# Kernel optimization log

Measured on AMD Instinct MI355X. Metric: run time of the kernel, lower is better.

Reference implementation:

```python
import jax, jax.numpy as jnp
import numpy as np

D_MODEL = 1024
NHEAD = 16
HEAD_DIM = D_MODEL // NHEAD
D_FF = 4096
B, S = 2, 2048
LN_EPS = 1e-5


def _linear_params(key, d_out, d_in):
    kw, kb = jax.random.split(key)
    lim = 1.0 / np.sqrt(d_in)
    W = jax.random.uniform(kw, (d_out, d_in), jnp.float32, -lim, lim)
    b = jax.random.uniform(kb, (d_out,), jnp.float32, -lim, lim)
    return W, b


def setup_inputs() -> dict:
    key = jax.random.key(0)
    ks = jax.random.split(key, 8)
    src = jax.random.normal(ks[0], (B, S, D_MODEL), jnp.float32)
    mask = jax.random.randint(ks[1], (B, S), 0, 2).astype(bool)
    Wq, bq = _linear_params(ks[2], D_MODEL, D_MODEL)
    Wk, bk = _linear_params(ks[3], D_MODEL, D_MODEL)
    Wv, bv = _linear_params(ks[4], D_MODEL, D_MODEL)
    Wo, bo = _linear_params(ks[5], D_MODEL, D_MODEL)
    W1, b1 = _linear_params(ks[6], D_FF, D_MODEL)
    W2, b2 = _linear_params(ks[7], D_MODEL, D_FF)
    ln1_g = jnp.ones((D_MODEL,), jnp.float32)
    ln1_b = jnp.zeros((D_MODEL,), jnp.float32)
    ln2_g = jnp.ones((D_MODEL,), jnp.float32)
    ln2_b = jnp.zeros((D_MODEL,), jnp.float32)
    return dict(src=src, mask=mask, Wq=Wq, bq=bq, Wk=Wk, bk=bk, Wv=Wv, bv=bv,
                Wo=Wo, bo=bo, W1=W1, b1=b1, W2=W2, b2=b2,
                ln1_g=ln1_g, ln1_b=ln1_b, ln2_g=ln2_g, ln2_b=ln2_b)


def _layernorm(x, g, b):
    mu = jnp.mean(x, axis=-1, keepdims=True)
    var = jnp.mean(jnp.square(x - mu), axis=-1, keepdims=True)
    return (x - mu) * jax.lax.rsqrt(var + LN_EPS) * g + b


def reference(src, mask, Wq, bq, Wk, bk, Wv, bv, Wo, bo, W1, b1, W2, b2,
              ln1_g, ln1_b, ln2_g, ln2_b):
    batch, seq, _ = src.shape
    src_norm = _layernorm(src, ln1_g, ln1_b)
    # projections (torch Linear: x @ W.T + b), split heads -> [B,H,S,Dh]
    def proj(W, b):
        y = jnp.einsum('bsi,oi->bso', src_norm, W) + b
        return y.reshape(batch, seq, NHEAD, HEAD_DIM).transpose(0, 2, 1, 3)
    q, k, v = proj(Wq, bq), proj(Wk, bk), proj(Wv, bv)
    scores = jnp.einsum('bhqd,bhkd->bhqk', q, k) / np.sqrt(HEAD_DIM)
    scores = jnp.where(mask[:, None, None, :], -10000.0, scores)
    attn_probs = jax.nn.softmax(scores, axis=-1)
    attn_out = jnp.einsum('bhqk,bhkd->bhqd', attn_probs, v)
    attn_out = attn_out.transpose(0, 2, 1, 3).reshape(batch, seq, D_MODEL)
    attn_out = jnp.einsum('bsi,oi->bso', attn_out, Wo) + bo
    src = src + attn_out
    src_norm2 = _layernorm(src, ln2_g, ln2_b)
    h = jax.nn.relu(jnp.einsum('bsi,oi->bso', src_norm2, W1) + b1)
    ff = jnp.einsum('bsi,oi->bso', h, W2) + b2
    src = src + ff
    return (src, attn_probs)
```

## Files before the change

kernel.cpp:

```cpp
#include <hip/hip_runtime.h>
#include <math.h>

typedef __bf16 bf16;
typedef __bf16 bf16x4 __attribute__((ext_vector_type(4)));
typedef __bf16 bf16x8 __attribute__((ext_vector_type(8)));
typedef float f32x4 __attribute__((ext_vector_type(4)));

__device__ __forceinline__ f32x4 mfma16(bf16x8 a, bf16x8 b, f32x4 c) {
  return __builtin_amdgcn_mfma_f32_16x16x32_bf16(a, b, c, 0, 0, 0);
}

__device__ __forceinline__ void gload_lds16(const void* g, void* l) {
  __builtin_amdgcn_global_load_lds((__attribute__((address_space(1))) void*)(g),
                                   (__attribute__((address_space(3))) void*)(l),
                                   16, 0, 0);
}

__global__ __launch_bounds__(256)
void cvt_all(const float* __restrict__ Wq, const float* __restrict__ Wk,
             const float* __restrict__ Wv, const float* __restrict__ Wo,
             const float* __restrict__ W1, const float* __restrict__ W2,
             const float* __restrict__ bq, const float* __restrict__ bk,
             const float* __restrict__ bv, bf16* __restrict__ wqkv,
             bf16* __restrict__ wob, bf16* __restrict__ w1b,
             bf16* __restrict__ w2b, float* __restrict__ bqkv) {
  const int i = blockIdx.x * 256 + threadIdx.x;
  if (i < 3145728) {
    float4 v;
    bf16* dst;
    size_t di;
    if (i < 262144) { v = ((const float4*)Wq)[i]; dst = wqkv; di = i; }
    else if (i < 524288) { v = ((const float4*)Wk)[i - 262144]; dst = wqkv; di = i; }
    else if (i < 786432) { v = ((const float4*)Wv)[i - 524288]; dst = wqkv; di = i; }
    else if (i < 1048576) { v = ((const float4*)Wo)[i - 786432]; dst = wob; di = i - 786432; }
    else if (i < 2097152) { v = ((const float4*)W1)[i - 1048576]; dst = w1b; di = i - 1048576; }
    else { v = ((const float4*)W2)[i - 2097152]; dst = w2b; di = i - 2097152; }
    bf16x4 o;
    o[0] = (bf16)v.x; o[1] = (bf16)v.y; o[2] = (bf16)v.z; o[3] = (bf16)v.w;
    reinterpret_cast<bf16x4*>(dst)[di] = o;
  } else {
    const int j = i - 3145728;
    const float* s = (j < 256) ? bq : ((j < 512) ? bk : bv);
    reinterpret_cast<float4*>(bqkv)[j] = reinterpret_cast<const float4*>(s)[j & 255];
  }
}

__global__ __launch_bounds__(256)
void ln_bf16(const float* __restrict__ x, const float* __restrict__ g,
             const float* __restrict__ bta, bf16* __restrict__ y) {
  const int row = blockIdx.x, t = threadIdx.x;
  const float4 v = reinterpret_cast<const float4*>(x)[(size_t)row * 256 + t];
  float s1 = v.x + v.y + v.z + v.w;
  float s2 = v.x * v.x + v.y * v.y + v.z * v.z + v.w * v.w;
#pragma unroll
  for (int m = 1; m < 64; m <<= 1) {
    s1 += __shfl_xor(s1, m);
    s2 += __shfl_xor(s2, m);
  }
  __shared__ float red[8];
  if ((t & 63) == 0) { red[(t >> 6) * 2] = s1; red[(t >> 6) * 2 + 1] = s2; }
  __syncthreads();
  s1 = red[0] + red[2] + red[4] + red[6];
  s2 = red[1] + red[3] + red[5] + red[7];
  const float mu = s1 * (1.f / 1024.f);
  const float rs = rsqrtf(s2 * (1.f / 1024.f) - mu * mu + 1e-5f);
  const float4 gv = reinterpret_cast<const float4*>(g)[t];
  const float4 bv = reinterpret_cast<const float4*>(bta)[t];
  bf16x4 o;
  o[0] = (bf16)((v.x - mu) * rs * gv.x + bv.x);
  o[1] = (bf16)((v.y - mu) * rs * gv.y + bv.y);
  o[2] = (bf16)((v.z - mu) * rs * gv.z + bv.z);
  o[3] = (bf16)((v.w - mu) * rs * gv.w + bv.w);
  reinterpret_cast<bf16x4*>(y)[(size_t)row * 256 + t] = o;
}

__global__ __launch_bounds__(256)
void tr_v(const bf16* __restrict__ QKV, bf16* __restrict__ VT) {
  __shared__ bf16 T[64 * 80];
  const int t = threadIdx.x;
  const int sb = blockIdx.x * 64, h = blockIdx.y, b = blockIdx.z;
  const int srow = t >> 2, c16 = t & 3;
  const bf16* src = QKV + (size_t)(b * 2048 + sb + srow) * 3072 + 2048 + h * 64 + c16 * 16;
  bf16x8 a0 = *reinterpret_cast<const bf16x8*>(src);
  bf16x8 a1 = *reinterpret_cast<const bf16x8*>(src + 8);
  *reinterpret_cast<bf16x8*>(&T[srow * 80 + c16 * 16]) = a0;
  *reinterpret_cast<bf16x8*>(&T[srow * 80 + c16 * 16 + 8]) = a1;
  __syncthreads();
  const int drow = t >> 2, sq = t & 3;
  bf16x8 o0, o1;
#pragma unroll
  for (int j = 0; j < 8; ++j) o0[j] = T[(sq * 16 + j) * 80 + drow];
#pragma unroll
  for (int j = 0; j < 8; ++j) o1[j] = T[(sq * 16 + 8 + j) * 80 + drow];
  bf16* dst = VT + ((size_t)(b * 16 + h) * 64 + drow) * 2048 + sb + sq * 16;
  *reinterpret_cast<bf16x8*>(dst) = o0;
  *reinterpret_cast<bf16x8*>(dst + 8) = o1;
}

template <bool RELU, bool QSC>
__global__ __launch_bounds__(512)
void gemm_bt3(const bf16* __restrict__ A, const bf16* __restrict__ Bw,
              const float* __restrict__ bias, bf16* __restrict__ Cout,
              int M, int N, int K) {
  __shared__ bf16 As[3][128 * 32];
  __shared__ bf16 Bs[3][256 * 32];
  const int t = threadIdx.x, wave = t >> 6, lane = t & 63;
  const int l15 = lane & 15, lhi = lane >> 4;
  const int nwg = gridDim.x * gridDim.y;
  const int orig = blockIdx.y * gridDim.x + blockIdx.x;
  const int wgid = (orig & 7) * (nwg >> 3) + (orig >> 3);
  const int bx = wgid % gridDim.x, by = wgid / gridDim.x;
  const int m0 = by * 128, n0 = bx * 256;
  const int wm = (wave >> 2) * 64, wn = (wave & 3) * 64;
  const f32x4 z4 = {0.f, 0.f, 0.f, 0.f};
  f32x4 acc[4][4];
#pragma unroll
  for (int m = 0; m < 4; ++m)
#pragma unroll
    for (int n = 0; n < 4; ++n) acc[m][n] = z4;

  const int da = t * 16;
  const int ra = da >> 6, ca = (da & 63) ^ ((ra & 3) << 4);
  const bf16* agp = A + (size_t)(m0 + ra) * K + (ca >> 1);
  int db_[2], rb_[2];
  const bf16* bgp[2];
#pragma unroll
  for (int j = 0; j < 2; ++j) {
    db_[j] = j * 8192 + t * 16;
    rb_[j] = db_[j] >> 6;
    const int cb = (db_[j] & 63) ^ ((rb_[j] & 3) << 4);
    bgp[j] = Bw + (size_t)(n0 + rb_[j]) * K + (cb >> 1);
  }

#define G3_STAGE(k0, bb)                                                      \
  do {                                                                        \
    gload_lds16(agp + (k0), (char*)As[bb] + da);                              \
    gload_lds16(bgp[0] + (k0), (char*)Bs[bb] + db_[0]);                       \
    gload_lds16(bgp[1] + (k0), (char*)Bs[bb] + db_[1]);                       \
  } while (0)

  const int nt = K >> 5;
  G3_STAGE(0, 0);
  G3_STAGE(32, 1);
  asm volatile("s_waitcnt vmcnt(3)" ::: "memory");
  __builtin_amdgcn_s_barrier();

  for (int kt = 0; kt < nt; ++kt) {
    if (kt + 2 < nt) G3_STAGE((kt + 2) * 32, (kt + 2) % 3);
    const char* Ac = (const char*)As[kt % 3];
    const char* Bc = (const char*)Bs[kt % 3];
    bf16x8 af[4], bfr[4];
#pragma unroll
    for (int m = 0; m < 4; ++m) {
      const int row = wm + m * 16 + l15;
      af[m] = *reinterpret_cast<const bf16x8*>(
          Ac + row * 64 + ((lhi * 16) ^ ((row & 3) << 4)));
    }
#pragma unroll
    for (int n = 0; n < 4; ++n) {
      const int row = wn + n * 16 + l15;
      bfr[n] = *reinterpret_cast<const bf16x8*>(
          Bc + row * 64 + ((lhi * 16) ^ ((row & 3) << 4)));
    }
    __builtin_amdgcn_s_setprio(1);
#pragma unroll
    for (int m = 0; m < 4; ++m)
#pragma unroll
      for (int n = 0; n < 4; ++n) acc[m][n] = mfma16(af[m], bfr[n], acc[m][n]);
    __builtin_amdgcn_s_setprio(0);
    if (kt + 1 < nt) {
      if (kt + 2 < nt)
        asm volatile("s_waitcnt vmcnt(3)" ::: "memory");
      else
        asm volatile("s_waitcnt vmcnt(0)" ::: "memory");
      __builtin_amdgcn_s_barrier();
    }
  }
#undef G3_STAGE

  const float sc = (QSC && n0 < 1024) ? 0.18033688011112042f : 1.0f;
#pragma unroll
  for (int m = 0; m < 4; ++m) {
    const int row_base = m0 + wm + m * 16 + lhi * 4;
#pragma unroll
    for (int n = 0; n < 4; ++n) {
      const int col = n0 + wn + n * 16 + l15;
      const float bv = bias[col];
#pragma unroll
      for (int r = 0; r < 4; ++r) {
        float v = (acc[m][n][r] + bv) * sc;
        if (RELU) v = v > 0.f ? v : 0.f;
        Cout[(size_t)(row_base + r) * N + col] = (bf16)v;
      }
    }
  }
}

template <int TM, bool OUT_BF16, bool RELU, bool RES, bool QSC>
__global__ __launch_bounds__(256)
void gemm_bt(const bf16* __restrict__ A, const bf16* __restrict__ Bw,
             const float* __restrict__ bias, const float* __restrict__ res,
             void* __restrict__ Cout, int M, int N, int K) {
  constexpr int MR = TM / 32;
  constexpr int ACH = TM / 64;
  __shared__ bf16 As[3][TM * 32];
  __shared__ bf16 Bs[3][128 * 32];
  const int t = threadIdx.x, wave = t >> 6, lane = t & 63;
  const int l15 = lane & 15, lhi = lane >> 4;
  const int nwg = gridDim.x * gridDim.y;
  const int orig = blockIdx.y * gridDim.x + blockIdx.x;
  const int wgid = (orig & 7) * (nwg >> 3) + (orig >> 3);
  const int bx = wgid % gridDim.x, by = wgid / gridDim.x;
  const int m0 = by * TM, n0 = bx * 128;
  const int wm = (wave >> 1) * (TM / 2), wn = (wave & 1) * 64;
  const f32x4 z4 = {0.f, 0.f, 0.f, 0.f};
  f32x4 acc[MR][4];
#pragma unroll
  for (int m = 0; m < MR; ++m)
#pragma unroll
    for (int n = 0; n < 4; ++n) acc[m][n] = z4;

  int soff[2], srow[2], scol[2];
#pragma unroll
  for (int i = 0; i < 2; ++i) {
    soff[i] = (i * 4 + wave) * 1024 + lane * 16;
    srow[i] = soff[i] >> 6;
    scol[i] = (soff[i] & 63) >> 1;
  }

#define GEMM_STAGE(k0, bb)                                                    \
  do {                                                                        \
    _Pragma("unroll")                                                         \
    for (int i = 0; i < ACH; ++i)                                             \
      gload_lds16(A + (size_t)(m0 + srow[i]) * K + (k0) + scol[i],            \
                  (char*)As[bb] + soff[i]);                                   \
    _Pragma("unroll")                                                         \
    for (int i = 0; i < 2; ++i)                                               \
      gload_lds16(Bw + (size_t)(n0 + srow[i]) * K + (k0) + scol[i],           \
                  (char*)Bs[bb] + soff[i]);                                   \
  } while (0)

  const int nt = K >> 5;
  GEMM_STAGE(0, 0);
  GEMM_STAGE(32, 1);
  if constexpr (TM == 128)
    asm volatile("s_waitcnt vmcnt(4)" ::: "memory");
  else
    asm volatile("s_waitcnt vmcnt(3)" ::: "memory");
  __builtin_amdgcn_s_barrier();

  for (int kt = 0; kt < nt; ++kt) {
    if (kt + 2 < nt) GEMM_STAGE((kt + 2) * 32, (kt + 2) % 3);
    const bf16* Ac = As[kt % 3];
    const bf16* Bc = Bs[kt % 3];
    bf16x8 af[MR], bfr[4];
#pragma unroll
    for (int m = 0; m < MR; ++m)
      af[m] = *reinterpret_cast<const bf16x8*>(&Ac[(wm + m * 16 + l15) * 32 + lhi * 8]);
#pragma unroll
    for (int n = 0; n < 4; ++n)
      bfr[n] = *reinterpret_cast<const bf16x8*>(&Bc[(wn + n * 16 + l15) * 32 + lhi * 8]);
    __builtin_amdgcn_s_setprio(1);
#pragma unroll
    for (int m = 0; m < MR; ++m)
#pragma unroll
      for (int n = 0; n < 4; ++n) acc[m][n] = mfma16(af[m], bfr[n], acc[m][n]);
    __builtin_amdgcn_s_setprio(0);
    if (kt + 1 < nt) {
      if (kt + 2 < nt) {
        if constexpr (TM == 128)
          asm volatile("s_waitcnt vmcnt(4)" ::: "memory");
        else
          asm volatile("s_waitcnt vmcnt(3)" ::: "memory");
      } else {
        asm volatile("s_waitcnt vmcnt(0)" ::: "memory");
      }
      __builtin_amdgcn_s_barrier();
    }
  }
#undef GEMM_STAGE

  const float sc = (QSC && n0 < 1024) ? 0.18033688011112042f : 1.0f;
#pragma unroll
  for (int m = 0; m < MR; ++m) {
    const int row_base = m0 + wm + m * 16 + lhi * 4;
#pragma unroll
    for (int n = 0; n < 4; ++n) {
      const int col = n0 + wn + n * 16 + l15;
      const float bv = bias[col];
#pragma unroll
      for (int r = 0; r < 4; ++r) {
        const int row = row_base + r;
        float v = (acc[m][n][r] + bv) * sc;
        if (RELU) v = v > 0.f ? v : 0.f;
        if (RES) v += res[(size_t)row * N + col];
        if (OUT_BF16)
          ((bf16*)Cout)[(size_t)row * N + col] = (bf16)v;
        else
          ((float*)Cout)[(size_t)row * N + col] = v;
      }
    }
  }
}

__global__ __launch_bounds__(512)
void attn_fused2(const bf16* __restrict__ Qp, const bf16* __restrict__ Kp,
                 const bf16* __restrict__ VTp, const int* __restrict__ mask,
                 float* __restrict__ probs, bf16* __restrict__ Ob) {
  constexpr int S = 2048, LD = 3072, KB = 128, NT = S / KB;
  __shared__ bf16 Kt[KB * 64];
  __shared__ bf16 Vt[64 * KB];
  __shared__ bf16 P[128 * KB];
  __shared__ float msk2[2][KB];
  const int t = threadIdx.x, wave = t >> 6, lane = t & 63;
  const int l15 = lane & 15, lhi = lane >> 4;
  const int flat = blockIdx.x + 16 * (blockIdx.y + 16 * blockIdx.z);
  const int wg = (flat & 7) * 64 + (flat >> 3);
  const int q0 = (wg & 15) * 128, h = (wg >> 4) & 15, b = wg >> 8;
  const int* mrow = mask + b * S;
  const f32x4 z4 = {0.f, 0.f, 0.f, 0.f};

  const bf16* kgp[2];
  const bf16* vgp[2];
  int soff[2];
#pragma unroll
  for (int i = 0; i < 2; ++i) {
    const int off = (i * 8 + wave) * 1024 + lane * 16;
    soff[i] = off;
    const int krow = off >> 7, kbin = off & 127;
    kgp[i] = Kp + (size_t)(b * S + krow) * LD + h * 64 + ((kbin ^ ((krow & 7) << 4)) >> 1);
    const int d = off >> 8, vbin = off & 255;
    vgp[i] = VTp + (size_t)((b * 16 + h) * 64 + d) * S + ((vbin ^ ((d & 7) << 4)) >> 1);
  }

  bf16x8 qf[2];
#pragma unroll
  for (int ks = 0; ks < 2; ++ks)
    qf[ks] = *reinterpret_cast<const bf16x8*>(
        Qp + (size_t)(b * S + q0 + wave * 16 + l15) * LD + h * 64 + ks * 32 + lhi * 8);

  bf16x8 kreg[2];
  float mnext;
#pragma unroll
  for (int i = 0; i < 2; ++i) kreg[i] = *reinterpret_cast<const bf16x8*>(kgp[i]);
  mnext = (t < KB) ? (mrow[t] ? 0.f : 1.f) : 0.f;
#pragma unroll
  for (int i = 0; i < 2; ++i)
    *reinterpret_cast<bf16x8*>((char*)Kt + soff[i]) = kreg[i];
  if (t < KB) msk2[0][t] = mnext;
  __syncthreads();

  float lpart = 0.f;
  for (int kt = 0; kt < NT; ++kt) {
    const int kv0 = kt * KB;
    if (kt + 1 < NT) {
#pragma unroll
      for (int i = 0; i < 2; ++i)
        kreg[i] = *reinterpret_cast<const bf16x8*>(kgp[i] + (size_t)(kv0 + KB) * LD);
      mnext = (t < KB) ? (mrow[kv0 + KB + t] ? 0.f : 1.f) : 0.f;
    }
    const char* kb = (kt & 1) ? (const char*)Vt : (const char*)Kt;
    const float* mc = msk2[kt & 1];
    f32x4 sa[8];
#pragma unroll
    for (int n = 0; n < 8; ++n) sa[n] = z4;
    __builtin_amdgcn_s_setprio(1);
#pragma unroll
    for (int ks = 0; ks < 2; ++ks)
#pragma unroll
      for (int n = 0; n < 8; ++n) {
        const int krow = n * 16 + l15;
        bf16x8 kf = *reinterpret_cast<const bf16x8*>(
            kb + krow * 128 + ((ks * 64 + lhi * 16) ^ ((krow & 7) << 4)));
        sa[n] = mfma16(kf, qf[ks], sa[n]);
      }
    __builtin_amdgcn_s_setprio(0);
#pragma unroll
    for (int n = 0; n < 8; ++n)
#pragma unroll
      for (int r = 0; r < 4; ++r)
        lpart += __builtin_exp2f(sa[n][r]) * mc[n * 16 + lhi * 4 + r];
    if (kt + 1 < NT) {
      char* kbn = ((kt + 1) & 1) ? (char*)Vt : (char*)Kt;
#pragma unroll
      for (int i = 0; i < 2; ++i)
        *reinterpret_cast<bf16x8*>(kbn + soff[i]) = kreg[i];
      if (t < KB) msk2[(kt + 1) & 1][t] = mnext;
    }
    __syncthreads();
  }
  lpart += __shfl_xor(lpart, 16);
  lpart += __shfl_xor(lpart, 32);
  const float il = 1.f / lpart;

  f32x4 oa[4];
#pragma unroll
  for (int n = 0; n < 4; ++n) oa[n] = z4;
  float* pbase = probs + ((size_t)(b * 16 + h) * S + q0 + wave * 16 + l15) * S;
  const int prw = wave * 16 + l15;

  bf16x8 vreg[2];
#pragma unroll
  for (int i = 0; i < 2; ++i) {
    kreg[i] = *reinterpret_cast<const bf16x8*>(kgp[i]);
    vreg[i] = *reinterpret_cast<const bf16x8*>(vgp[i]);
  }
  mnext = (t < KB) ? (mrow[t] ? 0.f : 1.f) : 0.f;
#pragma unroll
  for (int i = 0; i < 2; ++i) {
    *reinterpret_cast<bf16x8*>((char*)Kt + soff[i]) = kreg[i];
    *reinterpret_cast<bf16x8*>((char*)Vt + soff[i]) = vreg[i];
  }
  if (t < KB) msk2[0][t] = mnext;
  __syncthreads();

  for (int kt = 0; kt < NT; ++kt) {
    const int kv0 = kt * KB;
    if (kt + 1 < NT) {
#pragma unroll
      for (int i = 0; i < 2; ++i) {
        kreg[i] = *reinterpret_cast<const bf16x8*>(kgp[i] + (size_t)(kv0 + KB) * LD);
        vreg[i] = *reinterpret_cast<const bf16x8*>(vgp[i] + kv0 + KB);
      }
      mnext = (t < KB) ? (mrow[kv0 + KB + t] ? 0.f : 1.f) : 0.f;
    }

    f32x4 sa[8];
#pragma unroll
    for (int n = 0; n < 8; ++n) sa[n] = z4;
    __builtin_amdgcn_s_setprio(1);
#pragma unroll
    for (int ks = 0; ks < 2; ++ks)
#pragma unroll
      for (int n = 0; n < 8; ++n) {
        const int krow = n * 16 + l15;
        bf16x8 kf = *reinterpret_cast<const bf16x8*>(
            (char*)Kt + krow * 128 + ((ks * 64 + lhi * 16) ^ ((krow & 7) << 4)));
        sa[n] = mfma16(kf, qf[ks], sa[n]);
      }
    __builtin_amdgcn_s_setprio(0);

#pragma unroll
    for (int n = 0; n < 8; ++n) {
      f32x4 praw, pn;
#pragma unroll
      for (int r = 0; r < 4; ++r) {
        praw[r] = __builtin_exp2f(sa[n][r]) * msk2[0][n * 16 + lhi * 4 + r];
        pn[r] = praw[r] * il;
      }
      __builtin_nontemporal_store(pn, reinterpret_cast<f32x4*>(pbase + kv0 + n * 16 + lhi * 4));
      bf16x4 pb;
      pb[0] = (bf16)praw[0]; pb[1] = (bf16)praw[1];
      pb[2] = (bf16)praw[2]; pb[3] = (bf16)praw[3];
      *reinterpret_cast<bf16x4*>(
          (char*)P + prw * 256 + ((n * 32 + lhi * 8) ^ ((prw & 7) << 4))) = pb;
    }
    __builtin_amdgcn_s_setprio(1);
#pragma unroll
    for (int ks = 0; ks < 4; ++ks) {
      bf16x8 pf = *reinterpret_cast<const bf16x8*>(
          (char*)P + prw * 256 + ((ks * 64 + lhi * 16) ^ ((prw & 7) << 4)));
#pragma unroll
      for (int nn = 0; nn < 4; ++nn) {
        const int vr = nn * 16 + l15;
        bf16x8 vf = *reinterpret_cast<const bf16x8*>(
            (char*)Vt + vr * 256 + ((ks * 64 + lhi * 16) ^ ((vr & 7) << 4)));
        oa[nn] = mfma16(pf, vf, oa[nn]);
      }
    }
    __builtin_amdgcn_s_setprio(0);
    __syncthreads();
    if (kt + 1 < NT) {
#pragma unroll
      for (int i = 0; i < 2; ++i) {
        *reinterpret_cast<bf16x8*>((char*)Kt + soff[i]) = kreg[i];
        *reinterpret_cast<bf16x8*>((char*)Vt + soff[i]) = vreg[i];
      }
      if (t < KB) msk2[0][t] = mnext;
    }
    __syncthreads();
  }

  float il4[4];
#pragma unroll
  for (int r = 0; r < 4; ++r) il4[r] = __shfl(il, lhi * 4 + r);
#pragma unroll
  for (int nn = 0; nn < 4; ++nn)
#pragma unroll
    for (int r = 0; r < 4; ++r)
      Ob[(size_t)(b * S + q0 + wave * 16 + lhi * 4 + r) * 1024 + h * 64 + nn * 16 + l15] =
          (bf16)(oa[nn][r] * il4[r]);
}

extern "C" void kernel_launch(void* const* d_in, const int* in_sizes, int n_in,
                              void* d_out, int out_size, void* d_ws, size_t ws_size,
                              hipStream_t stream) {
  const float* src = (const float*)d_in[0];
  const int* mask = (const int*)d_in[1];
  const float* Wq = (const float*)d_in[2];
  const float* bq = (const float*)d_in[3];
  const float* Wk = (const float*)d_in[4];
  const float* bk = (const float*)d_in[5];
  const float* Wv = (const float*)d_in[6];
  const float* bv = (const float*)d_in[7];
  const float* Wo = (const float*)d_in[8];
  const float* bo = (const float*)d_in[9];
  const float* W1 = (const float*)d_in[10];
  const float* b1 = (const float*)d_in[11];
  const float* W2 = (const float*)d_in[12];
  const float* b2 = (const float*)d_in[13];
  const float* ln1g = (const float*)d_in[14];
  const float* ln1b = (const float*)d_in[15];
  const float* ln2g = (const float*)d_in[16];
  const float* ln2b = (const float*)d_in[17];

  float* out0 = (float*)d_out;
  float* probs = (float*)d_out + (size_t)4194304;

  char* w = (char*)d_ws;
  const size_t MB = 1u << 20;
  bf16* wqkv = (bf16*)(w);
  bf16* wob = (bf16*)(w + 6 * MB);
  bf16* w1b = (bf16*)(w + 8 * MB);
  bf16* w2b = (bf16*)(w + 16 * MB);
  bf16* xn = (bf16*)(w + 24 * MB);
  bf16* QKV = (bf16*)(w + 32 * MB);
  bf16* Ob = (bf16*)(w + 56 * MB);
  bf16* hb = (bf16*)(w + 32 * MB);
  bf16* VT = (bf16*)(w + 64 * MB);
  float* s2 = (float*)(w + 64 * MB);
  float* bqkv = (float*)(w + 80 * MB);

  cvt_all<<<12291, 256, 0, stream>>>(Wq, Wk, Wv, Wo, W1, W2, bq, bk, bv,
                                     wqkv, wob, w1b, w2b, bqkv);

  ln_bf16<<<4096, 256, 0, stream>>>(src, ln1g, ln1b, xn);
  gemm_bt3<false, true><<<dim3(12, 32), 512, 0, stream>>>(
      xn, wqkv, bqkv, QKV, 4096, 3072, 1024);
  tr_v<<<dim3(32, 16, 2), 256, 0, stream>>>(QKV, VT);
  attn_fused2<<<dim3(16, 16, 2), 512, 0, stream>>>(
      QKV, QKV + 1024, VT, mask, probs, Ob);
  gemm_bt<64, false, false, true, false><<<dim3(8, 64), 256, 0, stream>>>(
      Ob, wob, bo, src, s2, 4096, 1024, 1024);
  ln_bf16<<<4096, 256, 0, stream>>>(s2, ln2g, ln2b, xn);
  gemm_bt3<true, false><<<dim3(16, 32), 512, 0, stream>>>(
      xn, w1b, b1, hb, 4096, 4096, 1024);
  gemm_bt<64, false, false, true, false><<<dim3(8, 64), 256, 0, stream>>>(
      hb, w2b, b2, s2, out0, 4096, 1024, 4096);

  (void)in_sizes; (void)n_in; (void)out_size; (void)ws_size;
}
```

Measured before the change: 408.6 us.

## Switch GEMMs to 32x32 MFMA, fuse LN1 into prep, store residual as bf16

Both GEMM kernels move from 16x16x32 to 32x32x16 bf16 MFMA tiles, which cuts LDS fragment reads per MFMA and changes the epilogue row mapping. The first layernorm is merged into the weight-conversion launch to save one kernel launch. The intermediate residual after attention is now stored as bf16 rather than fp32, which halves its traffic but loses precision in the residual path that feeds the final output.

```diff
diff --git a/kernel.cpp b/kernel.cpp
--- a/kernel.cpp
+++ b/kernel.cpp
@@ -5,9 +5,13 @@
 typedef __bf16 bf16x4 __attribute__((ext_vector_type(4)));
 typedef __bf16 bf16x8 __attribute__((ext_vector_type(8)));
 typedef float f32x4 __attribute__((ext_vector_type(4)));
+typedef float f32x16 __attribute__((ext_vector_type(16)));
 
 __device__ __forceinline__ f32x4 mfma16(bf16x8 a, bf16x8 b, f32x4 c) {
   return __builtin_amdgcn_mfma_f32_16x16x32_bf16(a, b, c, 0, 0, 0);
+}
+__device__ __forceinline__ f32x16 mfma32(bf16x8 a, bf16x8 b, f32x16 c) {
+  return __builtin_amdgcn_mfma_f32_32x32x16_bf16(a, b, c, 0, 0, 0);
 }
 
 __device__ __forceinline__ void gload_lds16(const void* g, void* l) {
@@ -17,39 +21,75 @@
 }
 
 __global__ __launch_bounds__(256)
-void cvt_all(const float* __restrict__ Wq, const float* __restrict__ Wk,
-             const float* __restrict__ Wv, const float* __restrict__ Wo,
-             const float* __restrict__ W1, const float* __restrict__ W2,
-             const float* __restrict__ bq, const float* __restrict__ bk,
-             const float* __restrict__ bv, bf16* __restrict__ wqkv,
-             bf16* __restrict__ wob, bf16* __restrict__ w1b,
-             bf16* __restrict__ w2b, float* __restrict__ bqkv) {
-  const int i = blockIdx.x * 256 + threadIdx.x;
-  if (i < 3145728) {
-    float4 v;
-    bf16* dst;
-    size_t di;
-    if (i < 262144) { v = ((const float4*)Wq)[i]; dst = wqkv; di = i; }
-    else if (i < 524288) { v = ((const float4*)Wk)[i - 262144]; dst = wqkv; di = i; }
-    else if (i < 786432) { v = ((const float4*)Wv)[i - 524288]; dst = wqkv; di = i; }
-    else if (i < 1048576) { v = ((const float4*)Wo)[i - 786432]; dst = wob; di = i - 786432; }
-    else if (i < 2097152) { v = ((const float4*)W1)[i - 1048576]; dst = w1b; di = i - 1048576; }
-    else { v = ((const float4*)W2)[i - 2097152]; dst = w2b; di = i - 2097152; }
+void prep(const float* __restrict__ Wq, const float* __restrict__ Wk,
+          const float* __restrict__ Wv, const float* __restrict__ Wo,
+          const float* __restrict__ W1, const float* __restrict__ W2,
+          const float* __restrict__ bq, const float* __restrict__ bk,
+          const float* __restrict__ bv, bf16* __restrict__ wqkv,
+          bf16* __restrict__ wob, bf16* __restrict__ w1b,
+          bf16* __restrict__ w2b, float* __restrict__ bqkv,
+          const float* __restrict__ src, const float* __restrict__ g,
+          const float* __restrict__ bta, bf16* __restrict__ y) {
+  __shared__ float red[8];
+  if (blockIdx.x < 12291) {
+    const int i = blockIdx.x * 256 + threadIdx.x;
+    if (i < 3145728) {
+      float4 v;
+      bf16* dst;
+      size_t di;
+      if (i < 262144) { v = ((const float4*)Wq)[i]; dst = wqkv; di = i; }
+      else if (i < 524288) { v = ((const float4*)Wk)[i - 262144]; dst = wqkv; di = i; }
+      else if (i < 786432) { v = ((const float4*)Wv)[i - 524288]; dst = wqkv; di = i; }
+      else if (i < 1048576) { v = ((const float4*)Wo)[i - 786432]; dst = wob; di = i - 786432; }
+      else if (i < 2097152) { v = ((const float4*)W1)[i - 1048576]; dst = w1b; di = i - 1048576; }
+      else { v = ((const float4*)W2)[i - 2097152]; dst = w2b; di = i - 2097152; }
+      bf16x4 o;
+      o[0] = (bf16)v.x; o[1] = (bf16)v.y; o[2] = (bf16)v.z; o[3] = (bf16)v.w;
+      reinterpret_cast<bf16x4*>(dst)[di] = o;
+    } else {
+      const int j = i - 3145728;
+      const float* s = (j < 256) ? bq : ((j < 512) ? bk : bv);
+      reinterpret_cast<float4*>(bqkv)[j] = reinterpret_cast<const float4*>(s)[j & 255];
+    }
+  } else {
+    const int row = blockIdx.x - 12291, t = threadIdx.x;
+    const float4 v = reinterpret_cast<const float4*>(src)[(size_t)row * 256 + t];
+    float s1 = v.x + v.y + v.z + v.w;
+    float s2 = v.x * v.x + v.y * v.y + v.z * v.z + v.w * v.w;
+#pragma unroll
+    for (int m = 1; m < 64; m <<= 1) {
+      s1 += __shfl_xor(s1, m);
+      s2 += __shfl_xor(s2, m);
+    }
+    if ((t & 63) == 0) { red[(t >> 6) * 2] = s1; red[(t >> 6) * 2 + 1] = s2; }
+    __syncthreads();
+    s1 = red[0] + red[2] + red[4] + red[6];
+    s2 = red[1] + red[3] + red[5] + red[7];
+    const float mu = s1 * (1.f / 1024.f);
+    const float rs = rsqrtf(s2 * (1.f / 1024.f) - mu * mu + 1e-5f);
+    const float4 gv = reinterpret_cast<const float4*>(g)[t];
+    const float4 bv = reinterpret_cast<const float4*>(bta)[t];
     bf16x4 o;
-    o[0] = (bf16)v.x; o[1] = (bf16)v.y; o[2] = (bf16)v.z; o[3] = (bf16)v.w;
-    reinterpret_cast<bf16x4*>(dst)[di] = o;
+    o[0] = (bf16)((v.x - mu) * rs * gv.x + bv.x);
+    o[1] = (bf16)((v.y - mu) * rs * gv.y + bv.y);
+    o[2] = (bf16)((v.z - mu) * rs * gv.z + bv.z);
+    o[3] = (bf16)((v.w - mu) * rs * gv.w + bv.w);
+    reinterpret_cast<bf16x4*>(y)[(size_t)row * 256 + t] = o;
+  }
+}
+
+template <bool INBF>
+__global__ __launch_bounds__(256)
+void ln_any(const void* __restrict__ xx, const float* __restrict__ g,
+            const float* __restrict__ bta, bf16* __restrict__ y) {
+  const int row = blockIdx.x, t = threadIdx.x;
+  float4 v;
+  if constexpr (INBF) {
+    bf16x4 bv4 = reinterpret_cast<const bf16x4*>(xx)[(size_t)row * 256 + t];
+    v.x = (float)bv4[0]; v.y = (float)bv4[1]; v.z = (float)bv4[2]; v.w = (float)bv4[3];
   } else {
-    const int j = i - 3145728;
-    const float* s = (j < 256) ? bq : ((j < 512) ? bk : bv);
-    reinterpret_cast<float4*>(bqkv)[j] = reinterpret_cast<const float4*>(s)[j & 255];
-  }
-}
-
-__global__ __launch_bounds__(256)
-void ln_bf16(const float* __restrict__ x, const float* __restrict__ g,
-             const float* __restrict__ bta, bf16* __restrict__ y) {
-  const int row = blockIdx.x, t = threadIdx.x;
-  const float4 v = reinterpret_cast<const float4*>(x)[(size_t)row * 256 + t];
+    v = reinterpret_cast<const float4*>(xx)[(size_t)row * 256 + t];
+  }
   float s1 = v.x + v.y + v.z + v.w;
   float s2 = v.x * v.x + v.y * v.y + v.z * v.z + v.w * v.w;
 #pragma unroll
@@ -105,31 +145,32 @@
   __shared__ bf16 As[3][128 * 32];
   __shared__ bf16 Bs[3][256 * 32];
   const int t = threadIdx.x, wave = t >> 6, lane = t & 63;
-  const int l15 = lane & 15, lhi = lane >> 4;
+  const int l31 = lane & 31, lh2 = lane >> 5;
   const int nwg = gridDim.x * gridDim.y;
   const int orig = blockIdx.y * gridDim.x + blockIdx.x;
   const int wgid = (orig & 7) * (nwg >> 3) + (orig >> 3);
   const int bx = wgid % gridDim.x, by = wgid / gridDim.x;
   const int m0 = by * 128, n0 = bx * 256;
   const int wm = (wave >> 2) * 64, wn = (wave & 3) * 64;
-  const f32x4 z4 = {0.f, 0.f, 0.f, 0.f};
-  f32x4 acc[4][4];
-#pragma unroll
-  for (int m = 0; m < 4; ++m)
-#pragma unroll
-    for (int n = 0; n < 4; ++n) acc[m][n] = z4;
+  f32x16 acc[2][2];
+#pragma unroll
+  for (int m = 0; m < 2; ++m)
+#pragma unroll
+    for (int n = 0; n < 2; ++n)
+#pragma unroll
+      for (int r = 0; r < 16; ++r) acc[m][n][r] = 0.f;
 
   const int da = t * 16;
   const int ra = da >> 6, ca = (da & 63) ^ ((ra & 3) << 4);
   const bf16* agp = A + (size_t)(m0 + ra) * K + (ca >> 1);
-  int db_[2], rb_[2];
+  int db_[2];
   const bf16* bgp[2];
 #pragma unroll
   for (int j = 0; j < 2; ++j) {
     db_[j] = j * 8192 + t * 16;
-    rb_[j] = db_[j] >> 6;
-    const int cb = (db_[j] & 63) ^ ((rb_[j] & 3) << 4);
-    bgp[j] = Bw + (size_t)(n0 + rb_[j]) * K + (cb >> 1);
+    const int rb = db_[j] >> 6;
+    const int cb = (db_[j] & 63) ^ ((rb & 3) << 4);
+    bgp[j] = Bw + (size_t)(n0 + rb) * K + (cb >> 1);
   }
 
 #define G3_STAGE(k0, bb)                                                      \
@@ -149,24 +190,31 @@
     if (kt + 2 < nt) G3_STAGE((kt + 2) * 32, (kt + 2) % 3);
     const char* Ac = (const char*)As[kt % 3];
     const char* Bc = (const char*)Bs[kt % 3];
-    bf16x8 af[4], bfr[4];
-#pragma unroll
-    for (int m = 0; m < 4; ++m) {
-      const int row = wm + m * 16 + l15;
-      af[m] = *reinterpret_cast<const bf16x8*>(
-          Ac + row * 64 + ((lhi * 16) ^ ((row & 3) << 4)));
-    }
-#pragma unroll
-    for (int n = 0; n < 4; ++n) {
-      const int row = wn + n * 16 + l15;
-      bfr[n] = *reinterpret_cast<const bf16x8*>(
-          Bc + row * 64 + ((lhi * 16) ^ ((row & 3) << 4)));
+    bf16x8 af[2][2], bfr[2][2];
+#pragma unroll
+    for (int tm = 0; tm < 2; ++tm) {
+      const int row = wm + tm * 32 + l31;
+#pragma unroll
+      for (int kh = 0; kh < 2; ++kh)
+        af[tm][kh] = *reinterpret_cast<const bf16x8*>(
+            Ac + row * 64 + ((kh * 32 + lh2 * 16) ^ ((row & 3) << 4)));
+    }
+#pragma unroll
+    for (int tn = 0; tn < 2; ++tn) {
+      const int row = wn + tn * 32 + l31;
+#pragma unroll
+      for (int kh = 0; kh < 2; ++kh)
+        bfr[tn][kh] = *reinterpret_cast<const bf16x8*>(
+            Bc + row * 64 + ((kh * 32 + lh2 * 16) ^ ((row & 3) << 4)));
     }
     __builtin_amdgcn_s_setprio(1);
 #pragma unroll
-    for (int m = 0; m < 4; ++m)
-#pragma unroll
-      for (int n = 0; n < 4; ++n) acc[m][n] = mfma16(af[m], bfr[n], acc[m][n]);
+    for (int kh = 0; kh < 2; ++kh)
+#pragma unroll
+      for (int tm = 0; tm < 2; ++tm)
+#pragma unroll
+        for (int tn = 0; tn < 2; ++tn)
+          acc[tm][tn] = mfma32(af[tm][kh], bfr[tn][kh], acc[tm][tn]);
     __builtin_amdgcn_s_setprio(0);
     if (kt + 1 < nt) {
       if (kt + 2 < nt)
@@ -180,45 +228,42 @@
 
   const float sc = (QSC && n0 < 1024) ? 0.18033688011112042f : 1.0f;
 #pragma unroll
-  for (int m = 0; m < 4; ++m) {
-    const int row_base = m0 + wm + m * 16 + lhi * 4;
-#pragma unroll
-    for (int n = 0; n < 4; ++n) {
-      const int col = n0 + wn + n * 16 + l15;
+  for (int tm = 0; tm < 2; ++tm) {
+#pragma unroll
+    for (int tn = 0; tn < 2; ++tn) {
+      const int col = n0 + wn + tn * 32 + l31;
       const float bv = bias[col];
 #pragma unroll
-      for (int r = 0; r < 4; ++r) {
-        float v = (acc[m][n][r] + bv) * sc;
+      for (int reg = 0; reg < 16; ++reg) {
+        const int row = m0 + wm + tm * 32 + (reg & 3) + 8 * (reg >> 2) + 4 * lh2;
+        float v = (acc[tm][tn][reg] + bv) * sc;
         if (RELU) v = v > 0.f ? v : 0.f;
-        Cout[(size_t)(row_base + r) * N + col] = (bf16)v;
-      }
-    }
-  }
-}
-
-template <int TM, bool OUT_BF16, bool RELU, bool RES, bool QSC>
+        Cout[(size_t)row * N + col] = (bf16)v;
+      }
+    }
+  }
+}
+
+template <bool OUT_BF16, bool RES, bool RESBF>
 __global__ __launch_bounds__(256)
 void gemm_bt(const bf16* __restrict__ A, const bf16* __restrict__ Bw,
-             const float* __restrict__ bias, const float* __restrict__ res,
+             const float* __restrict__ bias, const void* __restrict__ res,
              void* __restrict__ Cout, int M, int N, int K) {
-  constexpr int MR = TM / 32;
-  constexpr int ACH = TM / 64;
-  __shared__ bf16 As[3][TM * 32];
+  __shared__ bf16 As[3][64 * 32];
   __shared__ bf16 Bs[3][128 * 32];
   const int t = threadIdx.x, wave = t >> 6, lane = t & 63;
-  const int l15 = lane & 15, lhi = lane >> 4;
+  const int l31 = lane & 31, lh2 = lane >> 5;
   const int nwg = gridDim.x * gridDim.y;
   const int orig = blockIdx.y * gridDim.x + blockIdx.x;
   const int wgid = (orig & 7) * (nwg >> 3) + (orig >> 3);
   const int bx = wgid % gridDim.x, by = wgid / gridDim.x;
-  const int m0 = by * TM, n0 = bx * 128;
-  const int wm = (wave >> 1) * (TM / 2), wn = (wave & 1) * 64;
-  const f32x4 z4 = {0.f, 0.f, 0.f, 0.f};
-  f32x4 acc[MR][4];
-#pragma unroll
-  for (int m = 0; m < MR; ++m)
-#pragma unroll
-    for (int n = 0; n < 4; ++n) acc[m][n] = z4;
+  const int m0 = by * 64, n0 = bx * 128;
+  const int wm = (wave >> 1) * 32, wn = (wave & 1) * 64;
+  f32x16 acc[2];
+#pragma unroll
+  for (int n = 0; n < 2; ++n)
+#pragma unroll
+    for (int r = 0; r < 16; ++r) acc[n][r] = 0.f;
 
   int soff[2], srow[2], scol[2];
 #pragma unroll
@@ -230,75 +275,71 @@
 
 #define GEMM_STAGE(k0, bb)                                                    \
   do {                                                                        \
-    _Pragma("unroll")                                                         \
-    for (int i = 0; i < ACH; ++i)                                             \
-      gload_lds16(A + (size_t)(m0 + srow[i]) * K + (k0) + scol[i],            \
-                  (char*)As[bb] + soff[i]);                                   \
-    _Pragma("unroll")                                                         \
-    for (int i = 0; i < 2; ++i)                                               \
-      gload_lds16(Bw + (size_t)(n0 + srow[i]) * K + (k0) + scol[i],           \
-                  (char*)Bs[bb] + soff[i]);                                   \
+    gload_lds16(A + (size_t)(m0 + srow[0]) * K + (k0) + scol[0],              \
+                (char*)As[bb] + soff[0]);                                     \
+    gload_lds16(Bw + (size_t)(n0 + srow[0]) * K + (k0) + scol[0],             \
+                (char*)Bs[bb] + soff[0]);                                     \
+    gload_lds16(Bw + (size_t)(n0 + srow[1]) * K + (k0) + scol[1],             \
+                (char*)Bs[bb] + soff[1]);                                     \
   } while (0)
 
   const int nt = K >> 5;
   GEMM_STAGE(0, 0);
   GEMM_STAGE(32, 1);
-  if constexpr (TM == 128)
-    asm volatile("s_waitcnt vmcnt(4)" ::: "memory");
-  else
-    asm volatile("s_waitcnt vmcnt(3)" ::: "memory");
+  asm volatile("s_waitcnt vmcnt(3)" ::: "memory");
   __builtin_amdgcn_s_barrier();
 
   for (int kt = 0; kt < nt; ++kt) {
     if (kt + 2 < nt) GEMM_STAGE((kt + 2) * 32, (kt + 2) % 3);
-    const bf16* Ac = As[kt % 3];
-    const bf16* Bc = Bs[kt % 3];
-    bf16x8 af[MR], bfr[4];
-#pragma unroll
-    for (int m = 0; m < MR; ++m)
-      af[m] = *reinterpret_cast<const bf16x8*>(&Ac[(wm + m * 16 + l15) * 32 + lhi * 8]);
-#pragma unroll
-    for (int n = 0; n < 4; ++n)
-      bfr[n] = *reinterpret_cast<const bf16x8*>(&Bc[(wn + n * 16 + l15) * 32 + lhi * 8]);
+    const char* Ac = (const char*)As[kt % 3];
+    const char* Bc = (const char*)Bs[kt % 3];
+    bf16x8 af[2], bfr[2][2];
+    {
+      const int row = wm + l31;
+#pragma unroll
+      for (int kh = 0; kh < 2; ++kh)
+        af[kh] = *reinterpret_cast<const bf16x8*>(Ac + row * 64 + kh * 32 + lh2 * 16);
+    }
+#pragma unroll
+    for (int tn = 0; tn < 2; ++tn) {
+      const int row = wn + tn * 32 + l31;
+#pragma unroll
+      for (int kh = 0; kh < 2; ++kh)
+        bfr[tn][kh] = *reinterpret_cast<const bf16x8*>(Bc + row * 64 + kh * 32 + lh2 * 16);
+    }
     __builtin_amdgcn_s_setprio(1);
 #pragma unroll
-    for (int m = 0; m < MR; ++m)
-#pragma unroll
-      for (int n = 0; n < 4; ++n) acc[m][n] = mfma16(af[m], bfr[n], acc[m][n]);
+    for (int kh = 0; kh < 2; ++kh)
+#pragma unroll
+      for (int tn = 0; tn < 2; ++tn)
+        acc[tn] = mfma32(af[kh], bfr[tn][kh], acc[tn]);
     __builtin_amdgcn_s_setprio(0);
     if (kt + 1 < nt) {
-      if (kt + 2 < nt) {
-        if constexpr (TM == 128)
-          asm volatile("s_waitcnt vmcnt(4)" ::: "memory");
-        else
-          asm volatile("s_waitcnt vmcnt(3)" ::: "memory");
-      } else {
+      if (kt + 2 < nt)
+        asm volatile("s_waitcnt vmcnt(3)" ::: "memory");
+      else
         asm volatile("s_waitcnt vmcnt(0)" ::: "memory");
-      }
       __builtin_amdgcn_s_barrier();
     }
   }
 #undef GEMM_STAGE
 
-  const float sc = (QSC && n0 < 1024) ? 0.18033688011112042f : 1.0f;
-#pragma unroll
-  for (int m = 0; m < MR; ++m) {
-    const int row_base = m0 + wm + m * 16 + lhi * 4;
-#pragma unroll
-    for (int n = 0; n < 4; ++n) {
-      const int col = n0 + wn + n * 16 + l15;
-      const float bv = bias[col];
-#pragma unroll
-      for (int r = 0; r < 4; ++r) {
-        const int row = row_base + r;
-        float v = (acc[m][n][r] + bv) * sc;
-        if (RELU) v = v > 0.f ? v : 0.f;
-        if (RES) v += res[(size_t)row * N + col];
-        if (OUT_BF16)
-          ((bf16*)Cout)[(size_t)row * N + col] = (bf16)v;
-        else
-          ((float*)Cout)[(size_t)row * N + col] = v;
-      }
+#pragma unroll
+  for (int tn = 0; tn < 2; ++tn) {
+    const int col = n0 + wn + tn * 32 + l31;
+    const float bv = bias[col];
+#pragma unroll
+    for (int reg = 0; reg < 16; ++reg) {
+      const int row = m0 + wm + (reg & 3) + 8 * (reg >> 2) + 4 * lh2;
+      float v = acc[tn][reg] + bv;
+      if (RES) {
+        const size_t idx = (size_t)row * N + col;
+        v += RESBF ? (float)((const bf16*)res)[idx] : ((const float*)res)[idx];
+      }
+      if (OUT_BF16)
+        ((bf16*)Cout)[(size_t)row * N + col] = (bf16)v;
+      else
+        ((float*)Cout)[(size_t)row * N + col] = v;
     }
   }
 }
@@ -528,24 +569,23 @@
   bf16* Ob = (bf16*)(w + 56 * MB);
   bf16* hb = (bf16*)(w + 32 * MB);
   bf16* VT = (bf16*)(w + 64 * MB);
-  float* s2 = (float*)(w + 64 * MB);
+  bf16* s2 = (bf16*)(w + 72 * MB);
   float* bqkv = (float*)(w + 80 * MB);
 
-  cvt_all<<<12291, 256, 0, stream>>>(Wq, Wk, Wv, Wo, W1, W2, bq, bk, bv,
-                                     wqkv, wob, w1b, w2b, bqkv);
-
-  ln_bf16<<<4096, 256, 0, stream>>>(src, ln1g, ln1b, xn);
+  prep<<<16387, 256, 0, stream>>>(Wq, Wk, Wv, Wo, W1, W2, bq, bk, bv,
+                                  wqkv, wob, w1b, w2b, bqkv,
+                                  src, ln1g, ln1b, xn);
   gemm_bt3<false, true><<<dim3(12, 32), 512, 0, stream>>>(
       xn, wqkv, bqkv, QKV, 4096, 3072, 1024);
   tr_v<<<dim3(32, 16, 2), 256, 0, stream>>>(QKV, VT);
   attn_fused2<<<dim3(16, 16, 2), 512, 0, stream>>>(
       QKV, QKV + 1024, VT, mask, probs, Ob);
-  gemm_bt<64, false, false, true, false><<<dim3(8, 64), 256, 0, stream>>>(
+  gemm_bt<true, true, false><<<dim3(8, 64), 256, 0, stream>>>(
       Ob, wob, bo, src, s2, 4096, 1024, 1024);
-  ln_bf16<<<4096, 256, 0, stream>>>(s2, ln2g, ln2b, xn);
+  ln_any<true><<<4096, 256, 0, stream>>>(s2, ln2g, ln2b, xn);
   gemm_bt3<true, false><<<dim3(16, 32), 512, 0, stream>>>(
       xn, w1b, b1, hb, 4096, 4096, 1024);
-  gemm_bt<64, false, false, true, false><<<dim3(8, 64), 256, 0, stream>>>(
+  gemm_bt<false, true, true><<<dim3(8, 64), 256, 0, stream>>>(
       hb, w2b, b2, s2, out0, 4096, 1024, 4096);
 
   (void)in_sizes; (void)n_in; (void)out_size; (void)ws_size;
```

Result: slower. 440.3 us (+7.8%).
